# Kernel tuning notes

Hardware: AMD Instinct MI355X
Metric: run time of the kernel (lower is better)

## Reference

```python
import jax, jax.numpy as jnp
import numpy as np
from jax.ops import segment_sum, segment_max

N_NODES = 50000
N_EDGES = 800000
B = 1024            # number of graphs
NODE_DIM = 21
ESM_DIM = 480
TAB_DIM = 7
H = 128             # hidden_dim
LSTM_H = H // 2     # 64 per direction
NEG_SLOPE = 0.2
BN_EPS = 1e-5


def setup_inputs() -> dict:
    key = jax.random.key(0)
    ks = iter(jax.random.split(key, 48))
    r = lambda shape, s=0.05: (s * jax.random.normal(next(ks), shape)).astype(jnp.float32)
    inp = {
        'x': jax.random.normal(next(ks), (N_NODES, NODE_DIM), dtype=jnp.float32),
        'edge_index': jax.random.randint(next(ks), (2, N_EDGES), 0, N_NODES, dtype=jnp.int64),
        'batch': jnp.sort(jax.random.randint(next(ks), (N_NODES,), 0, B, dtype=jnp.int64)),
        'esm_emb': jax.random.normal(next(ks), (B, ESM_DIM), dtype=jnp.float32),
        'tab_feats': jax.random.normal(next(ks), (B, TAB_DIM), dtype=jnp.float32),
        # GATConv 1 (heads=1)
        'gat1_W': r((H, NODE_DIM)), 'gat1_asrc': r((H,)), 'gat1_adst': r((H,)), 'gat1_b': r((H,)),
        # GATConv 2
        'gat2_W': r((H, H)), 'gat2_asrc': r((H,)), 'gat2_adst': r((H,)), 'gat2_b': r((H,)),
        # Bidirectional LSTM (seq_len=1, so a single cell step per direction)
        'lstm_Wih_f': r((4 * LSTM_H, ESM_DIM)), 'lstm_Whh_f': r((4 * LSTM_H, LSTM_H)),
        'lstm_bih_f': r((4 * LSTM_H,)), 'lstm_bhh_f': r((4 * LSTM_H,)),
        'lstm_Wih_r': r((4 * LSTM_H, ESM_DIM)), 'lstm_Whh_r': r((4 * LSTM_H, LSTM_H)),
        'lstm_bih_r': r((4 * LSTM_H,)), 'lstm_bhh_r': r((4 * LSTM_H,)),
        # tabular net
        'tab_W': r((64, TAB_DIM)), 'tab_b': r((64,)), 'tab_bn_g': jnp.ones((64,), jnp.float32), 'tab_bn_b': jnp.zeros((64,), jnp.float32),
        # fusion head
        'fus1_W': r((256, 320)), 'fus1_b': r((256,)), 'fus_bn_g': jnp.ones((256,), jnp.float32), 'fus_bn_b': jnp.zeros((256,), jnp.float32),
        'fus2_W': r((128, 256)), 'fus2_b': r((128,)),
        'fus3_W': r((1, 128)), 'fus3_b': r((1,)),
    }
    return inp


def _gat(h_in, src, dst, W, a_src, a_dst, bias):
    # PyG GATConv, heads=1, concat=True, self-loops already appended.
    h = h_in @ W.T                                  # [N, H]
    alpha_s = h @ a_src                             # [N]
    alpha_d = h @ a_dst                             # [N]
    e = jax.nn.leaky_relu(alpha_s[src] + alpha_d[dst], NEG_SLOPE)  # [E]
    m = segment_max(e, dst, num_segments=N_NODES)   # stable softmax per target
    ex = jnp.exp(e - m[dst])
    den = segment_sum(ex, dst, num_segments=N_NODES)
    coef = ex / (den[dst] + 1e-16)
    out = segment_sum(coef[:, None] * h[src], dst, num_segments=N_NODES)
    return out + bias


def _bn(x, g, b):
    # BatchNorm1d in training mode: biased batch statistics
    mu = jnp.mean(x, axis=0)
    var = jnp.var(x, axis=0)
    return (x - mu) * jax.lax.rsqrt(var + BN_EPS) * g + b


def _lstm_step(x, Wih, Whh, bih, bhh):
    # single step with zero initial (h, c); Whh term vanishes but kept for fidelity
    g = x @ Wih.T + bih + jnp.zeros((x.shape[0], Whh.shape[1]), x.dtype) @ Whh.T + bhh
    i, f, gg, o = jnp.split(g, 4, axis=1)           # PyTorch gate order i,f,g,o
    c = jax.nn.sigmoid(i) * jnp.tanh(gg)
    return jax.nn.sigmoid(o) * jnp.tanh(c)


def reference(x, edge_index, batch, esm_emb, tab_feats,
              gat1_W, gat1_asrc, gat1_adst, gat1_b,
              gat2_W, gat2_asrc, gat2_adst, gat2_b,
              lstm_Wih_f, lstm_Whh_f, lstm_bih_f, lstm_bhh_f,
              lstm_Wih_r, lstm_Whh_r, lstm_bih_r, lstm_bhh_r,
              tab_W, tab_b, tab_bn_g, tab_bn_b,
              fus1_W, fus1_b, fus_bn_g, fus_bn_b,
              fus2_W, fus2_b, fus3_W, fus3_b):
    sl = jnp.arange(N_NODES, dtype=edge_index.dtype)
    src = jnp.concatenate([edge_index[0], sl])      # add_self_loops=True default
    dst = jnp.concatenate([edge_index[1], sl])

    h1 = jax.nn.relu(_gat(x, src, dst, gat1_W, gat1_asrc, gat1_adst, gat1_b))
    h2 = jax.nn.relu(_gat(h1, src, dst, gat2_W, gat2_asrc, gat2_adst, gat2_b))

    counts = segment_sum(jnp.ones((N_NODES,), h2.dtype), batch, num_segments=B)
    graph_embed = segment_sum(h2, batch, num_segments=B) / jnp.maximum(counts, 1.0)[:, None]

    # bilstm over seq_len=1: output at last (only) step = concat(fwd, bwd)
    h_f = _lstm_step(esm_emb, lstm_Wih_f, lstm_Whh_f, lstm_bih_f, lstm_bhh_f)
    h_r = _lstm_step(esm_emb, lstm_Wih_r, lstm_Whh_r, lstm_bih_r, lstm_bhh_r)
    seq_embed = jnp.concatenate([h_f, h_r], axis=1)  # [B, 128]

    tab_embed = jax.nn.relu(_bn(tab_feats @ tab_W.T + tab_b, tab_bn_g, tab_bn_b))

    z = jnp.concatenate([graph_embed, seq_embed, tab_embed], axis=1)  # [B, 320]
    z = jax.nn.relu(_bn(z @ fus1_W.T + fus1_b, fus_bn_g, fus_bn_b))   # dropout: identity (eval)
    z = jax.nn.relu(z @ fus2_W.T + fus2_b)
    return z @ fus3_W.T + fus3_b                     # [B, 1]
```

## Files before the change

kernel.cpp:

```cpp
#include <hip/hip_runtime.h>
#include <hip/hip_bf16.h>

#define N_NODES 50000
#define N_PAD   50048
#define N_EDGES 800000
#define E_TOT   850000
#define NB      1024
#define ESM_DIM 480
#define HD      128
#define NBUCK   196
#define CAP     5120
#define EPB     1661
#define SC_BLK  512
#define CVT_BLK 256
#define BND_BLK 196
#define WC_BLK  16
#define TAB_BLK 4
#define G1B     782
#define LSTM_B  96
#define LG      384
#define AGG_GRID 12500
#define NL_BLK  512

typedef short short8 __attribute__((ext_vector_type(8)));
typedef unsigned short ushort8 __attribute__((ext_vector_type(8)));
typedef float f32x4 __attribute__((ext_vector_type(4)));

__device__ __forceinline__ float bf2f(unsigned int u) {
    union { unsigned int i; float f; } c; c.i = u << 16; return c.f;
}
__device__ __forceinline__ unsigned short f2bf(float f) {
    union { float f; unsigned int i; } c; c.f = f;
    unsigned int i = c.i;
    return (unsigned short)((i + 0x7FFFu + ((i >> 16) & 1u)) >> 16);
}
__device__ __forceinline__ void split2(float v, unsigned short& h, unsigned short& l) {
    h = f2bf(v);
    l = f2bf(v - bf2f(h));
}


__device__ void dev_scatter(const int* __restrict__ ei, int* __restrict__ gcur,
                            int* __restrict__ pairs, int blk) {
    __shared__ int hist[NBUCK];
    int t = threadIdx.x;
    for (int u = t; u < NBUCK; u += 256) hist[u] = 0;
    __syncthreads();
    int e0 = blk * EPB;
    int e1 = (e0 + EPB < E_TOT) ? e0 + EPB : E_TOT;
    for (int e = e0 + t; e < e1; e += 256) {
        int d = (e < N_EDGES) ? ei[N_EDGES + e] : (e - N_EDGES);
        atomicAdd(&hist[d >> 8], 1);
    }
    __syncthreads();
    for (int u = t; u < NBUCK; u += 256) {
        int c = hist[u];
        hist[u] = (c > 0) ? atomicAdd(&gcur[u], c) : 0;
    }
    __syncthreads();
    for (int e = e0 + t; e < e1; e += 256) {
        int s, d;
        if (e < N_EDGES) { s = ei[e]; d = ei[N_EDGES + e]; }
        else             { s = d = e - N_EDGES; }
        int bu = d >> 8;
        int pos = atomicAdd(&hist[bu], 1);
        pairs[bu * CAP + pos] = s | ((d & 255) << 16);
    }
}

__device__ void dev_cvt(const float* __restrict__ esm,
                        const float* __restrict__ Wf,
                        const float* __restrict__ Wr,
                        const float* __restrict__ W1,
                        unsigned short* __restrict__ esm_h, unsigned short* __restrict__ esm_l,
                        unsigned short* __restrict__ wg_h,  unsigned short* __restrict__ wg_l,
                        unsigned short* __restrict__ w1h,   unsigned short* __restrict__ w1l,
                        int blk) {
    int tid = blk * 256 + threadIdx.x;
    for (int u = tid; u < NB * 120; u += CVT_BLK * 256) {
        float4 v = ((const float4*)esm)[u];
        ushort4 h, l;
        split2(v.x, h.x, l.x); split2(v.y, h.y, l.y);
        split2(v.z, h.z, l.z); split2(v.w, h.w, l.w);
        ((ushort4*)esm_h)[u] = h; ((ushort4*)esm_l)[u] = l;
    }
    for (int u = tid; u < LG * 120; u += CVT_BLK * 256) {
        int n = u / 120, kk = u - n * 120;
        int rr = (n >= 192) ? n - 192 : n;
        const float* Ws = (n >= 192) ? Wr : Wf;
        int srow = (rr < 64) ? rr : rr + 64;
        float4 v = *(const float4*)&Ws[(size_t)srow * 480 + kk * 4];
        ushort4 h, l;
        split2(v.x, h.x, l.x); split2(v.y, h.y, l.y);
        split2(v.z, h.z, l.z); split2(v.w, h.w, l.w);
        ((ushort4*)wg_h)[u] = h; ((ushort4*)wg_l)[u] = l;
    }
    for (int u = tid; u < 128 * 32; u += CVT_BLK * 256) {
        int f = u >> 5, k = u & 31;
        float v = (k < 21) ? W1[f * 21 + k] : 0.f;
        unsigned short h, l;
        split2(v, h, l);
        w1h[u] = h; w1l[u] = l;
    }
}

__device__ void dev_tab4(const float* __restrict__ tf, const float* __restrict__ W,
                         const float* __restrict__ bias, const float* __restrict__ g,
                         const float* __restrict__ b, float* __restrict__ z, int blk) {
    __shared__ float ssum[16][16];
    __shared__ float ssq[16][16];
    int t = threadIdx.x;
    int rg = t >> 4, jl = t & 15;
    int j = blk * 16 + jl;
    float Wj[7];
#pragma unroll
    for (int k = 0; k < 7; ++k) Wj[k] = W[j * 7 + k];
    float bj = bias[j];
    float s = 0.f, q = 0.f;
    for (int rr = 0; rr < 64; ++rr) {
        int row = rg * 64 + rr;
        const float* xp = &tf[(size_t)row * 7];
        float a = bj;
#pragma unroll
        for (int k = 0; k < 7; ++k) a += xp[k] * Wj[k];
        s += a; q += a * a;
    }
    ssum[rg][jl] = s; ssq[rg][jl] = q;
    __syncthreads();
    for (int off = 8; off; off >>= 1) {
        if (rg < off) { ssum[rg][jl] += ssum[rg + off][jl]; ssq[rg][jl] += ssq[rg + off][jl]; }
        __syncthreads();
    }
    float mu = ssum[0][jl] * (1.f / 1024.f);
    float var = ssq[0][jl] * (1.f / 1024.f) - mu * mu;
    float sc = rsqrtf(var + 1e-5f) * g[j];
    float sh = b[j] - mu * sc;
    for (int rr = 0; rr < 64; ++rr) {
        int row = rg * 64 + rr;
        const float* xp = &tf[(size_t)row * 7];
        float a = bj;
#pragma unroll
        for (int k = 0; k < 7; ++k) a += xp[k] * Wj[k];
        z[(size_t)row * 320 + 256 + j] = fmaxf(a * sc + sh, 0.f);
    }
}

__global__ __launch_bounds__(256) void megaA(
        const int* __restrict__ ei, int* __restrict__ gcur, int* __restrict__ pairs,
        const float* __restrict__ esm, const float* __restrict__ Wih_f,
        const float* __restrict__ Wih_r, const float* __restrict__ gat1_W,
        unsigned short* __restrict__ esm_h, unsigned short* __restrict__ esm_l,
        unsigned short* __restrict__ wg_h,  unsigned short* __restrict__ wg_l,
        unsigned short* __restrict__ w1h,   unsigned short* __restrict__ w1l,
        const int* __restrict__ batch, int* __restrict__ gstart,
        const float* __restrict__ W2, unsigned short* __restrict__ Wb,
        const float* __restrict__ tf, const float* __restrict__ tab_W,
        const float* __restrict__ tab_b, const float* __restrict__ tab_g,
        const float* __restrict__ tab_bb, float* __restrict__ z) {
    int b = blockIdx.x, t = threadIdx.x;
    if (b < SC_BLK) {
        dev_scatter(ei, gcur, pairs, b);
    } else if (b < SC_BLK + CVT_BLK) {
        dev_cvt(esm, Wih_f, Wih_r, gat1_W, esm_h, esm_l, wg_h, wg_l, w1h, w1l, b - SC_BLK);
    } else if (b < SC_BLK + CVT_BLK + BND_BLK) {
        int i = (b - (SC_BLK + CVT_BLK)) * 256 + t;
        if (i >= N_NODES) return;
        int bb = batch[i];
        int bp = (i == 0) ? -1 : batch[i - 1];
        for (int g = bp + 1; g <= bb; ++g) gstart[g] = i;
        if (i == N_NODES - 1)
            for (int g = bb + 1; g <= NB; ++g) gstart[g] = N_NODES;
    } else if (b < SC_BLK + CVT_BLK + BND_BLK + WC_BLK) {
        int i = (b - (SC_BLK + CVT_BLK + BND_BLK)) * 256 + t;
        if (i >= 128 * 32) return;
        float4 v = ((const float4*)W2)[i];
        ((ushort4*)Wb)[i] = make_ushort4(f2bf(v.x), f2bf(v.y), f2bf(v.z), f2bf(v.w));
    } else {
        dev_tab4(tf, tab_W, tab_b, tab_g, tab_bb, z,
                 b - (SC_BLK + CVT_BLK + BND_BLK + WC_BLK));
    }
}


__device__ __forceinline__ float sigmoidf_(float x) { return 1.f / (1.f + __expf(-x)); }

__device__ void dev_gat1_mfma(const float* __restrict__ X,
                              const unsigned short* __restrict__ w1h,
                              const unsigned short* __restrict__ w1l,
                              const float* __restrict__ asrc, const float* __restrict__ adst,
                              unsigned short* __restrict__ out,
                              float* __restrict__ alpha_s, float* __restrict__ alpha_d,
                              int blk) {
    int t = threadIdx.x;
    int wid = t >> 6, L = t & 63, quad = L >> 4, lo = L & 15;
    int m0 = blk * 64 + wid * 16;
    int row = m0 + lo;
    const float* xr = X + (size_t)row * 21;
    int kbase = quad * 8;
    bool valid = row < N_NODES;
    float xv[8];
#pragma unroll
    for (int j = 0; j < 8; ++j) {
        int k = kbase + j;
        xv[j] = (valid && k < 21) ? xr[k] : 0.f;
    }
    short8 ah, al;
#pragma unroll
    for (int j = 0; j < 8; ++j) {
        unsigned short h, l;
        split2(xv[j], h, l);
        ah[j] = (short)h; al[j] = (short)l;
    }
    float as_p[4] = {0.f, 0.f, 0.f, 0.f};
    float ad_p[4] = {0.f, 0.f, 0.f, 0.f};
#pragma unroll
    for (int ft = 0; ft < 8; ++ft) {
        short8 bh = *(const short8*)&w1h[(ft * 16 + lo) * 32 + kbase];
        short8 bl = *(const short8*)&w1l[(ft * 16 + lo) * 32 + kbase];
        f32x4 acc = {0.f, 0.f, 0.f, 0.f};
        acc = __builtin_amdgcn_mfma_f32_16x16x32_bf16(ah, bh, acc, 0, 0, 0);
        acc = __builtin_amdgcn_mfma_f32_16x16x32_bf16(al, bh, acc, 0, 0, 0);
        acc = __builtin_amdgcn_mfma_f32_16x16x32_bf16(ah, bl, acc, 0, 0, 0);
        float asv = asrc[ft * 16 + lo];
        float adv = adst[ft * 16 + lo];
#pragma unroll
        for (int r = 0; r < 4; ++r) {
            int m = m0 + quad * 4 + r;
            out[(size_t)m * HD + ft * 16 + lo] = f2bf(acc[r]);
            as_p[r] += acc[r] * asv;
            ad_p[r] += acc[r] * adv;
        }
    }
#pragma unroll
    for (int off = 1; off < 16; off <<= 1) {
#pragma unroll
        for (int r = 0; r < 4; ++r) {
            as_p[r] += __shfl_xor(as_p[r], off);
            ad_p[r] += __shfl_xor(ad_p[r], off);
        }
    }
    if (lo == 0) {
#pragma unroll
        for (int r = 0; r < 4; ++r) {
            int m = m0 + quad * 4 + r;
            if (m < N_NODES) { alpha_s[m] = as_p[r]; alpha_d[m] = ad_p[r]; }
        }
    }
}

__device__ void dev_lstm_mfma(const unsigned short* __restrict__ Ah,
                              const unsigned short* __restrict__ Al,
                              const unsigned short* __restrict__ Bh,
                              const unsigned short* __restrict__ Bl,
                              float* __restrict__ G, int blk) {
    __shared__ unsigned short Bsh[64][104];
    __shared__ unsigned short Bsl[64][104];
    int t = threadIdx.x;
    int wid = t >> 6, L = t & 63, quad = L >> 4, lo = L & 15;
    int nt = blk % 6, mt = blk / 6;
    int m0 = mt * 64 + wid * 16;
    int n0 = nt * 64;
    f32x4 accs[4];
#pragma unroll
    for (int ft = 0; ft < 4; ++ft) accs[ft] = (f32x4){0.f, 0.f, 0.f, 0.f};
    const unsigned short* arh = Ah + (size_t)(m0 + lo) * ESM_DIM;
    const unsigned short* arl = Al + (size_t)(m0 + lo) * ESM_DIM;
    for (int c = 0; c < 5; ++c) {
        int k0c = c * 96;
        short8 ah[3], al[3];
#pragma unroll
        for (int ks = 0; ks < 3; ++ks) {
            ah[ks] = *(const short8*)&arh[k0c + ks * 32 + quad * 8];
            al[ks] = *(const short8*)&arl[k0c + ks * 32 + quad * 8];
        }
#pragma unroll
        for (int u = 0; u < 3; ++u) {
            int li = u * 2048 + t * 8;
            int row = li / 96, col = li % 96;
            *(ushort8*)&Bsh[row][col] =
                *(const ushort8*)&Bh[(size_t)(n0 + row) * ESM_DIM + k0c + col];
            *(ushort8*)&Bsl[row][col] =
                *(const ushort8*)&Bl[(size_t)(n0 + row) * ESM_DIM + k0c + col];
        }
        __syncthreads();
#pragma unroll
        for (int ks = 0; ks < 3; ++ks) {
#pragma unroll
            for (int ft = 0; ft < 4; ++ft) {
                short8 bh = *(const short8*)&Bsh[ft * 16 + lo][ks * 32 + quad * 8];
                short8 bl = *(const short8*)&Bsl[ft * 16 + lo][ks * 32 + quad * 8];
                accs[ft] = __builtin_amdgcn_mfma_f32_16x16x32_bf16(ah[ks], bh, accs[ft], 0, 0, 0);
                accs[ft] = __builtin_amdgcn_mfma_f32_16x16x32_bf16(al[ks], bh, accs[ft], 0, 0, 0);
                accs[ft] = __builtin_amdgcn_mfma_f32_16x16x32_bf16(ah[ks], bl, accs[ft], 0, 0, 0);
            }
        }
        __syncthreads();
    }
#pragma unroll
    for (int ft = 0; ft < 4; ++ft) {
#pragma unroll
        for (int r = 0; r < 4; ++r)
            G[(size_t)(m0 + quad * 4 + r) * LG + n0 + ft * 16 + lo] = accs[ft][r];
    }
}

__global__ __launch_bounds__(256) void megaB(
        const int* __restrict__ gcur, const int* __restrict__ pairs,
        int* __restrict__ row_beg, int* __restrict__ row_end, int* __restrict__ csr_src,
        const float* __restrict__ x,
        const unsigned short* __restrict__ w1h, const unsigned short* __restrict__ w1l,
        const float* __restrict__ gat1_as, const float* __restrict__ gat1_ad,
        unsigned short* __restrict__ h0, float* __restrict__ alpha_s, float* __restrict__ alpha_d,
        const unsigned short* __restrict__ esm_h, const unsigned short* __restrict__ esm_l,
        const unsigned short* __restrict__ wg_h,  const unsigned short* __restrict__ wg_l,
        float* __restrict__ g_lstm) {
    int b = blockIdx.x, t = threadIdx.x;
    if (b < NBUCK) {
        __shared__ int dc[256];
        __shared__ int wt[4];
        __shared__ int cur[256];
        int rs = b * CAP;
        int re = rs + gcur[b];
        dc[t] = 0;
        __syncthreads();
        for (int i = rs + t; i < re; i += 1024) {
            int i1 = i + 256, i2 = i + 512, i3 = i + 768;
            int p0 = pairs[i];
            int p1 = (i1 < re) ? pairs[i1] : 0;
            int p2 = (i2 < re) ? pairs[i2] : 0;
            int p3 = (i3 < re) ? pairs[i3] : 0;
            atomicAdd(&dc[p0 >> 16], 1);
            if (i1 < re) atomicAdd(&dc[p1 >> 16], 1);
            if (i2 < re) atomicAdd(&dc[p2 >> 16], 1);
            if (i3 < re) atomicAdd(&dc[p3 >> 16], 1);
        }
        __syncthreads();
        int v = dc[t];
        int lane = t & 63, wid = t >> 6;
        int sc = v;
#pragma unroll
        for (int off = 1; off < 64; off <<= 1) {
            int n = __shfl_up(sc, off);
            if (lane >= off) sc += n;
        }
        if (lane == 63) wt[wid] = sc;
        __syncthreads();
        int pref = 0;
        for (int ww = 0; ww < wid; ++ww) pref += wt[ww];
        int beg = rs + pref + sc - v;
        int node = b * 256 + t;
        if (node < N_NODES) { row_beg[node] = beg; row_end[node] = beg + v; }
        cur[t] = beg;
        __syncthreads();
        for (int i = rs + t; i < re; i += 1024) {
            int i1 = i + 256, i2 = i + 512, i3 = i + 768;
            int p0 = pairs[i];
            int p1 = (i1 < re) ? pairs[i1] : 0;
            int p2 = (i2 < re) ? pairs[i2] : 0;
            int p3 = (i3 < re) ? pairs[i3] : 0;
            int pos0 = atomicAdd(&cur[p0 >> 16], 1);
            csr_src[pos0] = p0 & 0xFFFF;
            if (i1 < re) { int pos = atomicAdd(&cur[p1 >> 16], 1); csr_src[pos] = p1 & 0xFFFF; }
            if (i2 < re) { int pos = atomicAdd(&cur[p2 >> 16], 1); csr_src[pos] = p2 & 0xFFFF; }
            if (i3 < re) { int pos = atomicAdd(&cur[p3 >> 16], 1); csr_src[pos] = p3 & 0xFFFF; }
        }
    } else if (b < NBUCK + LSTM_B) {
        dev_lstm_mfma(esm_h, esm_l, wg_h, wg_l, g_lstm, b - NBUCK);
    } else {
        dev_gat1_mfma(x, w1h, w1l, gat1_as, gat1_ad, h0, alpha_s, alpha_d,
                      b - (NBUCK + LSTM_B));
    }
}


__global__ __launch_bounds__(256) void gemm_mfma(const unsigned short* __restrict__ A,
                                                 const unsigned short* __restrict__ Wb,
                                                 const float* __restrict__ asrc,
                                                 const float* __restrict__ adst,
                                                 unsigned short* __restrict__ out,
                                                 float* __restrict__ alpha_s,
                                                 float* __restrict__ alpha_d, int M) {
    __shared__ unsigned short Wlds[128 * 136];
    int t = threadIdx.x;
    for (int u = t; u < 128 * 16; u += 256) {
        int row = u >> 4, seg = u & 15;
        *(ushort8*)&Wlds[row * 136 + seg * 8] = *(const ushort8*)&Wb[row * 128 + seg * 8];
    }
    __syncthreads();
    int wid = t >> 6, L = t & 63;
    int quad = L >> 4, lo = L & 15;
    int m0 = blockIdx.x * 64 + wid * 16;
    short8 afrag[4];
#pragma unroll
    for (int ch = 0; ch < 4; ++ch)
        afrag[ch] = *(const short8*)&A[(size_t)(m0 + lo) * HD + ch * 32 + quad * 8];
    float as_p[4] = {0.f, 0.f, 0.f, 0.f};
    float ad_p[4] = {0.f, 0.f, 0.f, 0.f};
#pragma unroll
    for (int ft = 0; ft < 8; ++ft) {
        f32x4 acc = {0.f, 0.f, 0.f, 0.f};
#pragma unroll
        for (int ch = 0; ch < 4; ++ch) {
            short8 b = *(const short8*)&Wlds[(ft * 16 + lo) * 136 + ch * 32 + quad * 8];
            acc = __builtin_amdgcn_mfma_f32_16x16x32_bf16(afrag[ch], b, acc, 0, 0, 0);
        }
        float asv = asrc[ft * 16 + lo];
        float adv = adst[ft * 16 + lo];
#pragma unroll
        for (int r = 0; r < 4; ++r) {
            int m = m0 + quad * 4 + r;
            if (m < M) out[(size_t)m * HD + ft * 16 + lo] = f2bf(acc[r]);
            as_p[r] += acc[r] * asv;
            ad_p[r] += acc[r] * adv;
        }
    }
#pragma unroll
    for (int off = 1; off < 16; off <<= 1) {
#pragma unroll
        for (int r = 0; r < 4; ++r) {
            as_p[r] += __shfl_xor(as_p[r], off);
            ad_p[r] += __shfl_xor(ad_p[r], off);
        }
    }
    if (lo == 0) {
#pragma unroll
        for (int r = 0; r < 4; ++r) {
            int m = m0 + quad * 4 + r;
            if (m < M) { alpha_s[m] = as_p[r]; alpha_d[m] = ad_p[r]; }
        }
    }
}


__global__ void gat_spmm(const unsigned short* __restrict__ h, const int* __restrict__ row_beg,
                         const int* __restrict__ row_end, const int* __restrict__ csr_src,
                         const float* __restrict__ alpha_s, const float* __restrict__ alpha_d,
                         const float* __restrict__ bias, unsigned short* __restrict__ outp,
                         const float* __restrict__ g_lstm,
                         const float* __restrict__ bihf, const float* __restrict__ bhhf,
                         const float* __restrict__ bihr, const float* __restrict__ bhhr,
                         float* __restrict__ z) {
    if (blockIdx.x >= AGG_GRID) {
        int idx = (blockIdx.x - AGG_GRID) * 256 + threadIdx.x;
        int bb = idx >> 7, jj = idx & 127;
        int dir = jj >> 6, j = jj & 63;
        const float* gb = g_lstm + (size_t)bb * LG + dir * 192;
        const float* bi = dir ? bihr : bihf;
        const float* bh = dir ? bhhr : bhhf;
        float gi = gb[j]        + bi[j]        + bh[j];
        float gg = gb[64 + j]   + bi[128 + j]  + bh[128 + j];
        float go = gb[128 + j]  + bi[192 + j]  + bh[192 + j];
        float c = sigmoidf_(gi) * tanhf(gg);
        z[(size_t)bb * 320 + 128 + jj] = sigmoidf_(go) * tanhf(c);
        return;
    }
    int w = (int)((blockIdx.x * (size_t)blockDim.x + threadIdx.x) >> 6);
    int lane = threadIdx.x & 63;
    if (w >= N_NODES) return;
    int grp = lane >> 4, l16 = lane & 15;
    int rs = row_beg[w], re = row_end[w];
    int deg = re - rs;
    float ad = alpha_d[w];
    float acc[8] = {0.f, 0.f, 0.f, 0.f, 0.f, 0.f, 0.f, 0.f};
    if (deg <= 64) {
        int s_reg = 0;
        float e = -1e30f;
        if (lane < deg) {
            s_reg = csr_src[rs + lane];
            float t0 = alpha_s[s_reg] + ad;
            e = (t0 > 0.f) ? t0 : 0.2f * t0;
        }
        float m = e;
#pragma unroll
        for (int off = 32; off; off >>= 1) m = fmaxf(m, __shfl_xor(m, off));
        float ex = (lane < deg) ? __expf(e - m) : 0.f;
        float den = ex;
#pragma unroll
        for (int off = 32; off; off >>= 1) den += __shfl_xor(den, off);
        float coef = ex / (den + 1e-16f);
        int i = rs + grp;
        for (; i + 12 < re; i += 16) {
            int idx = i - rs;
            float c0 = __shfl(coef, idx);       int s0 = __shfl(s_reg, idx);
            float c1 = __shfl(coef, idx + 4);   int s1 = __shfl(s_reg, idx + 4);
            float c2 = __shfl(coef, idx + 8);   int s2 = __shfl(s_reg, idx + 8);
            float c3 = __shfl(coef, idx + 12);  int s3 = __shfl(s_reg, idx + 12);
            ushort8 h0 = *(const ushort8*)&h[(size_t)s0 * HD + l16 * 8];
            ushort8 h1 = *(const ushort8*)&h[(size_t)s1 * HD + l16 * 8];
            ushort8 h2 = *(const ushort8*)&h[(size_t)s2 * HD + l16 * 8];
            ushort8 h3 = *(const ushort8*)&h[(size_t)s3 * HD + l16 * 8];
#pragma unroll
            for (int j = 0; j < 8; ++j) acc[j] += c0 * bf2f(h0[j]);
#pragma unroll
            for (int j = 0; j < 8; ++j) acc[j] += c1 * bf2f(h1[j]);
#pragma unroll
            for (int j = 0; j < 8; ++j) acc[j] += c2 * bf2f(h2[j]);
#pragma unroll
            for (int j = 0; j < 8; ++j) acc[j] += c3 * bf2f(h3[j]);
        }
        for (; i < re; i += 4) {
            int idx = i - rs;
            float c0 = __shfl(coef, idx);
            int   s0 = __shfl(s_reg, idx);
            ushort8 h0 = *(const ushort8*)&h[(size_t)s0 * HD + l16 * 8];
#pragma unroll
            for (int j = 0; j < 8; ++j) acc[j] += c0 * bf2f(h0[j]);
        }
    } else {
        float m = -1e30f;
        for (int i = rs + lane; i < re; i += 64) {
            int s = csr_src[i];
            float t0 = alpha_s[s] + ad;
            t0 = (t0 > 0.f) ? t0 : 0.2f * t0;
            m = fmaxf(m, t0);
        }
#pragma unroll
        for (int off = 32; off; off >>= 1) m = fmaxf(m, __shfl_xor(m, off));
        float den = 0.f;
        for (int i = rs + lane; i < re; i += 64) {
            int s = csr_src[i];
            float t0 = alpha_s[s] + ad;
            t0 = (t0 > 0.f) ? t0 : 0.2f * t0;
            den += __expf(t0 - m);
        }
#pragma unroll
        for (int off = 32; off; off >>= 1) den += __shfl_xor(den, off);
        float inv = 1.f / (den + 1e-16f);
        for (int i = rs + grp; i < re; i += 4) {
            int s = csr_src[i];
            float t0 = alpha_s[s] + ad;
            t0 = (t0 > 0.f) ? t0 : 0.2f * t0;
            float c = __expf(t0 - m) * inv;
            ushort8 hv = *(const ushort8*)&h[(size_t)s * HD + l16 * 8];
#pragma unroll
            for (int j = 0; j < 8; ++j) acc[j] += c * bf2f(hv[j]);
        }
    }
#pragma unroll
    for (int j = 0; j < 8; ++j) {
        acc[j] += __shfl_xor(acc[j], 16);
        acc[j] += __shfl_xor(acc[j], 32);
    }
    int f0 = l16 * 8 + grp * 2;
    float2 bv = *(const float2*)&bias[f0];
    float vx = fmaxf(acc[grp * 2]     + bv.x, 0.f);
    float vy = fmaxf(acc[grp * 2 + 1] + bv.y, 0.f);
    unsigned int pv = (unsigned int)f2bf(vx) | ((unsigned int)f2bf(vy) << 16);
    *(unsigned int*)&outp[(size_t)w * HD + f0] = pv;
}


__global__ void pool_kernel(const unsigned short* __restrict__ h, const int* __restrict__ start,
                            float* __restrict__ z) {
    int w = (int)((blockIdx.x * (size_t)blockDim.x + threadIdx.x) >> 6);
    int lane = threadIdx.x & 63;
    if (w >= NB) return;
    int grp = lane >> 4, l16 = lane & 15;
    int s0 = start[w], s1 = start[w + 1];
    float acc[8] = {0.f, 0.f, 0.f, 0.f, 0.f, 0.f, 0.f, 0.f};
    int n = s0 + grp;
    for (; n + 4 < s1; n += 8) {
        ushort8 a = *(const ushort8*)&h[(size_t)n * HD + l16 * 8];
        ushort8 b = *(const ushort8*)&h[(size_t)(n + 4) * HD + l16 * 8];
#pragma unroll
        for (int j = 0; j < 8; ++j) acc[j] += bf2f(a[j]);
#pragma unroll
        for (int j = 0; j < 8; ++j) acc[j] += bf2f(b[j]);
    }
    if (n < s1) {
        ushort8 a = *(const ushort8*)&h[(size_t)n * HD + l16 * 8];
#pragma unroll
        for (int j = 0; j < 8; ++j) acc[j] += bf2f(a[j]);
    }
#pragma unroll
    for (int j = 0; j < 8; ++j) {
        acc[j] += __shfl_xor(acc[j], 16);
        acc[j] += __shfl_xor(acc[j], 32);
    }
    float inv = 1.f / fmaxf((float)(s1 - s0), 1.f);
    int f0 = l16 * 8 + grp * 2;
    *(float2*)&z[(size_t)w * 320 + f0] =
        make_float2(acc[grp * 2] * inv, acc[grp * 2 + 1] * inv);
}


__global__ __launch_bounds__(256) void fus1_mfma(const float* __restrict__ X,
                                                 const float* __restrict__ W1,
                                                 float* __restrict__ out,
                                                 float* __restrict__ colsum,
                                                 float* __restrict__ colsq) {
    __shared__ unsigned short Bsh[64][72];
    __shared__ unsigned short Bsl[64][72];
    __shared__ float cls[64], clq[64];
    int t = threadIdx.x;
    int wid = t >> 6, L = t & 63, quad = L >> 4, lo = L & 15;
    int m0 = blockIdx.x * 64 + wid * 16;
    int n0 = blockIdx.y * 64;
    if (t < 64) { cls[t] = 0.f; clq[t] = 0.f; }
    f32x4 accs[4];
#pragma unroll
    for (int ft = 0; ft < 4; ++ft) accs[ft] = (f32x4){0.f, 0.f, 0.f, 0.f};
    const float* ar = X + (size_t)(m0 + lo) * 320;
    for (int c = 0; c < 5; ++c) {
        int k0 = c * 64;
        short8 ah[2], al[2];
#pragma unroll
        for (int ks = 0; ks < 2; ++ks) {
            const float* ap = &ar[k0 + ks * 32 + quad * 8];
            float4 v0 = *(const float4*)ap;
            float4 v1 = *(const float4*)(ap + 4);
            float av[8] = {v0.x, v0.y, v0.z, v0.w, v1.x, v1.y, v1.z, v1.w};
#pragma unroll
            for (int j = 0; j < 8; ++j) {
                unsigned short hh, ll;
                split2(av[j], hh, ll);
                ah[ks][j] = (short)hh; al[ks][j] = (short)ll;
            }
        }
#pragma unroll
        for (int u = 0; u < 4; ++u) {
            int li = u * 256 + t;
            int row = li >> 4, col = (li & 15) * 4;
            float4 v = *(const float4*)&W1[(size_t)(n0 + row) * 320 + k0 + col];
            ushort4 hh, ll;
            split2(v.x, hh.x, ll.x); split2(v.y, hh.y, ll.y);
            split2(v.z, hh.z, ll.z); split2(v.w, hh.w, ll.w);
            *(ushort4*)&Bsh[row][col] = hh;
            *(ushort4*)&Bsl[row][col] = ll;
        }
        __syncthreads();
#pragma unroll
        for (int ks = 0; ks < 2; ++ks) {
#pragma unroll
            for (int ft = 0; ft < 4; ++ft) {
                short8 bh = *(const short8*)&Bsh[ft * 16 + lo][ks * 32 + quad * 8];
                short8 bl = *(const short8*)&Bsl[ft * 16 + lo][ks * 32 + quad * 8];
                accs[ft] = __builtin_amdgcn_mfma_f32_16x16x32_bf16(ah[ks], bh, accs[ft], 0, 0, 0);
                accs[ft] = __builtin_amdgcn_mfma_f32_16x16x32_bf16(al[ks], bh, accs[ft], 0, 0, 0);
                accs[ft] = __builtin_amdgcn_mfma_f32_16x16x32_bf16(ah[ks], bl, accs[ft], 0, 0, 0);
            }
        }
        __syncthreads();
    }
#pragma unroll
    for (int ft = 0; ft < 4; ++ft) {
        float s = 0.f, q = 0.f;
#pragma unroll
        for (int r = 0; r < 4; ++r) {
            float v = accs[ft][r];
            out[(size_t)(m0 + quad * 4 + r) * 256 + n0 + ft * 16 + lo] = v;
            s += v; q += v * v;
        }
        s += __shfl_xor(s, 16); s += __shfl_xor(s, 32);
        q += __shfl_xor(q, 16); q += __shfl_xor(q, 32);
        if (quad == 0) {
            atomicAdd(&cls[ft * 16 + lo], s);
            atomicAdd(&clq[ft * 16 + lo], q);
        }
    }
    __syncthreads();
    if (t < 64) {
        atomicAdd(&colsum[n0 + t], cls[t]);
        atomicAdd(&colsq[n0 + t],  clq[t]);
    }
}


__global__ __launch_bounds__(256) void fus2_mfma(const float* __restrict__ z1pre,
                                                 const float* __restrict__ colsum,
                                                 const float* __restrict__ colsq,
                                                 const float* __restrict__ fus_g,
                                                 const float* __restrict__ fus_bb,
                                                 const float* __restrict__ W2,
                                                 const float* __restrict__ b2,
                                                 const float* __restrict__ W3,
                                                 const float* __restrict__ b3,
                                                 float* __restrict__ out) {
    __shared__ unsigned short Bsh[128][72];
    __shared__ unsigned short Bsl[128][72];
    __shared__ float sc_[256], sh_[256];
    int t = threadIdx.x;
    {
        float mu = colsum[t] * (1.f / 1024.f);
        float var = colsq[t] * (1.f / 1024.f) - mu * mu;
        float s = rsqrtf(var + 1e-5f) * fus_g[t];
        sc_[t] = s;
        sh_[t] = fus_bb[t] - mu * s;
    }
    __syncthreads();
    int wid = t >> 6, L = t & 63, quad = L >> 4, lo = L & 15;
    int m0 = blockIdx.x * 64 + wid * 16;
    f32x4 accs[8];
#pragma unroll
    for (int ft = 0; ft < 8; ++ft) accs[ft] = (f32x4){0.f, 0.f, 0.f, 0.f};
    const float* ar = z1pre + (size_t)(m0 + lo) * 256;
    for (int c = 0; c < 4; ++c) {
        int k0 = c * 64;
        short8 ah[2], al[2];
#pragma unroll
        for (int ks = 0; ks < 2; ++ks) {
            int kb = k0 + ks * 32 + quad * 8;
            float4 v0 = *(const float4*)&ar[kb];
            float4 v1 = *(const float4*)&ar[kb + 4];
            float av[8] = {v0.x, v0.y, v0.z, v0.w, v1.x, v1.y, v1.z, v1.w};
#pragma unroll
            for (int j = 0; j < 8; ++j) {
                float xv = fmaxf(av[j] * sc_[kb + j] + sh_[kb + j], 0.f);
                unsigned short hh, ll;
                split2(xv, hh, ll);
                ah[ks][j] = (short)hh; al[ks][j] = (short)ll;
            }
        }
#pragma unroll
        for (int u = 0; u < 8; ++u) {
            int li = u * 256 + t;
            int row = li >> 4, col = (li & 15) * 4;
            float4 v = *(const float4*)&W2[(size_t)row * 256 + k0 + col];
            ushort4 hh, ll;
            split2(v.x, hh.x, ll.x); split2(v.y, hh.y, ll.y);
            split2(v.z, hh.z, ll.z); split2(v.w, hh.w, ll.w);
            *(ushort4*)&Bsh[row][col] = hh;
            *(ushort4*)&Bsl[row][col] = ll;
        }
        __syncthreads();
#pragma unroll
        for (int ks = 0; ks < 2; ++ks) {
#pragma unroll
            for (int ft = 0; ft < 8; ++ft) {
                short8 bh = *(const short8*)&Bsh[ft * 16 + lo][ks * 32 + quad * 8];
                short8 bl = *(const short8*)&Bsl[ft * 16 + lo][ks * 32 + quad * 8];
                accs[ft] = __builtin_amdgcn_mfma_f32_16x16x32_bf16(ah[ks], bh, accs[ft], 0, 0, 0);
                accs[ft] = __builtin_amdgcn_mfma_f32_16x16x32_bf16(al[ks], bh, accs[ft], 0, 0, 0);
                accs[ft] = __builtin_amdgcn_mfma_f32_16x16x32_bf16(ah[ks], bl, accs[ft], 0, 0, 0);
            }
        }
        __syncthreads();
    }
    float b3v = b3[0];
    float b2v[8], w3v[8];
#pragma unroll
    for (int ft = 0; ft < 8; ++ft) {
        int col = ft * 16 + lo;
        b2v[ft] = b2[col];
        w3v[ft] = W3[col];
    }
#pragma unroll
    for (int r = 0; r < 4; ++r) {
        float rsum = 0.f;
#pragma unroll
        for (int ft = 0; ft < 8; ++ft)
            rsum += fmaxf(accs[ft][r] + b2v[ft], 0.f) * w3v[ft];
        rsum += __shfl_xor(rsum, 1);
        rsum += __shfl_xor(rsum, 2);
        rsum += __shfl_xor(rsum, 4);
        rsum += __shfl_xor(rsum, 8);
        if (lo == 0) out[m0 + quad * 4 + r] = rsum + b3v;
    }
}


extern "C" void kernel_launch(void* const* d_in, const int* in_sizes, int n_in,
                              void* d_out, int out_size, void* d_ws, size_t ws_size,
                              hipStream_t stream) {
    const float* x        = (const float*)d_in[0];
    const int*   ei       = (const int*)d_in[1];
    const int*   batch    = (const int*)d_in[2];
    const float* esm      = (const float*)d_in[3];
    const float* tabf     = (const float*)d_in[4];
    const float* gat1_W   = (const float*)d_in[5];
    const float* gat1_as  = (const float*)d_in[6];
    const float* gat1_ad  = (const float*)d_in[7];
    const float* gat1_b   = (const float*)d_in[8];
    const float* gat2_W   = (const float*)d_in[9];
    const float* gat2_as  = (const float*)d_in[10];
    const float* gat2_ad  = (const float*)d_in[11];
    const float* gat2_b   = (const float*)d_in[12];
    const float* Wih_f    = (const float*)d_in[13];
    const float* bih_f    = (const float*)d_in[15];
    const float* bhh_f    = (const float*)d_in[16];
    const float* Wih_r    = (const float*)d_in[17];
    const float* bih_r    = (const float*)d_in[19];
    const float* bhh_r    = (const float*)d_in[20];
    const float* tab_W    = (const float*)d_in[21];
    const float* tab_b    = (const float*)d_in[22];
    const float* tab_g    = (const float*)d_in[23];
    const float* tab_bb   = (const float*)d_in[24];
    const float* fus1_W   = (const float*)d_in[25];
    const float* fus_g    = (const float*)d_in[27];
    const float* fus_bb   = (const float*)d_in[28];
    const float* fus2_W   = (const float*)d_in[29];
    const float* fus2_b   = (const float*)d_in[30];
    const float* fus3_W   = (const float*)d_in[31];
    const float* fus3_b   = (const float*)d_in[32];
    float* out = (float*)d_out;

    char* ws = (char*)d_ws;
    size_t off = 0;
    auto alloc = [&](size_t bytes) -> char* {
        char* p = ws + off;
        off += (bytes + 255) & ~(size_t)255;
        return p;
    };
    unsigned short* h0_bf = (unsigned short*)alloc((size_t)N_PAD * HD * 2);
    unsigned short* hA_bf = (unsigned short*)alloc((size_t)N_PAD * HD * 2);
    unsigned short* h2_bf = (unsigned short*)alloc((size_t)N_PAD * HD * 2);
    unsigned short* h_act = (unsigned short*)alloc((size_t)N_NODES * HD * 2);
    float* alpha_s = (float*)alloc((size_t)N_NODES * 4);
    float* alpha_d = (float*)alloc((size_t)N_NODES * 4);
    unsigned short* w2bf = (unsigned short*)alloc((size_t)HD * HD * 2);
    int*   row_beg = (int*)alloc((size_t)N_NODES * 4);
    int*   row_end = (int*)alloc((size_t)N_NODES * 4);
    int*   csr_src = (int*)alloc((size_t)NBUCK * CAP * 4);
    int*   pairs   = (int*)alloc((size_t)NBUCK * CAP * 4);
    int*   gstart  = (int*)alloc((size_t)(NB + 1) * 4);
    float* z1pre   = (float*)alloc((size_t)NB * 256 * 4);
    float* z       = (float*)alloc((size_t)NB * 320 * 4);
    float* g_lstm  = (float*)alloc((size_t)NB * LG * 4);
    unsigned short* esm_h = (unsigned short*)alloc((size_t)NB * ESM_DIM * 2);
    unsigned short* esm_l = (unsigned short*)alloc((size_t)NB * ESM_DIM * 2);
    unsigned short* wg_h  = (unsigned short*)alloc((size_t)LG * ESM_DIM * 2);
    unsigned short* wg_l  = (unsigned short*)alloc((size_t)LG * ESM_DIM * 2);
    unsigned short* w1h   = (unsigned short*)alloc((size_t)128 * 32 * 2);
    unsigned short* w1l   = (unsigned short*)alloc((size_t)128 * 32 * 2);
    int*   gcur    = (int*)alloc((size_t)NBUCK * 4);
    float* colsum  = (float*)alloc((size_t)256 * 4);
    float* colsq   = (float*)alloc((size_t)256 * 4);
    size_t zero_len = (size_t)((char*)colsq + 256 * 4 - (char*)gcur);
    hipMemsetAsync(gcur, 0, zero_len, stream);

    megaA<<<SC_BLK + CVT_BLK + BND_BLK + WC_BLK + TAB_BLK, 256, 0, stream>>>(
        ei, gcur, pairs, esm, Wih_f, Wih_r, gat1_W,
        esm_h, esm_l, wg_h, wg_l, w1h, w1l,
        batch, gstart, gat2_W, w2bf,
        tabf, tab_W, tab_b, tab_g, tab_bb, z);

    megaB<<<NBUCK + LSTM_B + G1B, 256, 0, stream>>>(
        gcur, pairs, row_beg, row_end, csr_src,
        x, w1h, w1l, gat1_as, gat1_ad, h0_bf, alpha_s, alpha_d,
        esm_h, esm_l, wg_h, wg_l, g_lstm);

    gat_spmm<<<AGG_GRID + NL_BLK, 256, 0, stream>>>(h0_bf, row_beg, row_end, csr_src,
                                                    alpha_s, alpha_d, gat1_b, hA_bf,
                                                    g_lstm, bih_f, bhh_f, bih_r, bhh_r, z);

    gemm_mfma<<<N_PAD / 64, 256, 0, stream>>>(hA_bf, w2bf, gat2_as, gat2_ad,
                                              h2_bf, alpha_s, alpha_d, N_NODES);

    gat_spmm<<<AGG_GRID, 256, 0, stream>>>(h2_bf, row_beg, row_end, csr_src,
                                           alpha_s, alpha_d, gat2_b, h_act,
                                           g_lstm, bih_f, bhh_f, bih_r, bhh_r, z);

    pool_kernel<<<(NB + 3) / 4, 256, 0, stream>>>(h_act, gstart, z);

    fus1_mfma<<<dim3(16, 4), 256, 0, stream>>>(z, fus1_W, z1pre, colsum, colsq);

    fus2_mfma<<<16, 256, 0, stream>>>(z1pre, colsum, colsq, fus_g, fus_bb,
                                      fus2_W, fus2_b, fus3_W, fus3_b, out);

    (void)in_sizes; (void)n_in; (void)out_size; (void)ws_size;
}
```

Before: 279.7 us.

## Fuse mean pooling into second GAT aggregation via atomics, retune scatter blocks

Layer-2 aggregation now does graph mean pooling itself. Each block stages its four output rows in shared memory, pre-scales them by 1/count, merges runs of rows that belong to the same graph and atomically adds the result into z. This drops the separate pool kernel and the bf16 activation buffer it read and wrote, at the cost of float atomics and a block-wide sync per block. z is now zeroed by the memset, and atomic summation makes the pooled result order-dependent. The tail gather loop is also unrolled by two, and the edge-scatter stage uses half as many blocks with twice the edges each.

```diff
diff --git a/kernel.cpp b/kernel.cpp
--- a/kernel.cpp
+++ b/kernel.cpp
@@ -10,8 +10,8 @@
 #define HD      128
 #define NBUCK   196
 #define CAP     5120
-#define EPB     1661
-#define SC_BLK  512
+#define EPB     3321
+#define SC_BLK  256
 #define CVT_BLK 256
 #define BND_BLK 196
 #define WC_BLK  16
@@ -439,7 +439,9 @@
                          const float* __restrict__ g_lstm,
                          const float* __restrict__ bihf, const float* __restrict__ bhhf,
                          const float* __restrict__ bihr, const float* __restrict__ bhhr,
-                         float* __restrict__ z) {
+                         float* __restrict__ z,
+                         const int* __restrict__ batch, const int* __restrict__ gstart,
+                         int do_pool) {
     if (blockIdx.x >= AGG_GRID) {
         int idx = (blockIdx.x - AGG_GRID) * 256 + threadIdx.x;
         int bb = idx >> 7, jj = idx & 127;
@@ -453,6 +455,14 @@
         float c = sigmoidf_(gi) * tanhf(gg);
         z[(size_t)bb * 320 + 128 + jj] = sigmoidf_(go) * tanhf(c);
         return;
+    }
+    __shared__ float rowbuf[4][128];
+    __shared__ int   gids[4];
+    __shared__ float invs[4];
+    if (do_pool && threadIdx.x < 4) {
+        int g = batch[blockIdx.x * 4 + threadIdx.x];
+        gids[threadIdx.x] = g;
+        invs[threadIdx.x] = 1.f / fmaxf((float)(gstart[g + 1] - gstart[g]), 1.f);
     }
     int w = (int)((blockIdx.x * (size_t)blockDim.x + threadIdx.x) >> 6);
     int lane = threadIdx.x & 63;
@@ -498,7 +508,18 @@
 #pragma unroll
             for (int j = 0; j < 8; ++j) acc[j] += c3 * bf2f(h3[j]);
         }
-        for (; i < re; i += 4) {
+        for (; i + 4 < re; i += 8) {
+            int idx = i - rs;
+            float c0 = __shfl(coef, idx);       int s0 = __shfl(s_reg, idx);
+            float c1 = __shfl(coef, idx + 4);   int s1 = __shfl(s_reg, idx + 4);
+            ushort8 h0 = *(const ushort8*)&h[(size_t)s0 * HD + l16 * 8];
+            ushort8 h1 = *(const ushort8*)&h[(size_t)s1 * HD + l16 * 8];
+#pragma unroll
+            for (int j = 0; j < 8; ++j) acc[j] += c0 * bf2f(h0[j]);
+#pragma unroll
+            for (int j = 0; j < 8; ++j) acc[j] += c1 * bf2f(h1[j]);
+        }
+        if (i < re) {
             int idx = i - rs;
             float c0 = __shfl(coef, idx);
             int   s0 = __shfl(s_reg, idx);
@@ -545,42 +566,29 @@
     float2 bv = *(const float2*)&bias[f0];
     float vx = fmaxf(acc[grp * 2]     + bv.x, 0.f);
     float vy = fmaxf(acc[grp * 2 + 1] + bv.y, 0.f);
-    unsigned int pv = (unsigned int)f2bf(vx) | ((unsigned int)f2bf(vy) << 16);
-    *(unsigned int*)&outp[(size_t)w * HD + f0] = pv;
-}
-
-
-__global__ void pool_kernel(const unsigned short* __restrict__ h, const int* __restrict__ start,
-                            float* __restrict__ z) {
-    int w = (int)((blockIdx.x * (size_t)blockDim.x + threadIdx.x) >> 6);
-    int lane = threadIdx.x & 63;
-    if (w >= NB) return;
-    int grp = lane >> 4, l16 = lane & 15;
-    int s0 = start[w], s1 = start[w + 1];
-    float acc[8] = {0.f, 0.f, 0.f, 0.f, 0.f, 0.f, 0.f, 0.f};
-    int n = s0 + grp;
-    for (; n + 4 < s1; n += 8) {
-        ushort8 a = *(const ushort8*)&h[(size_t)n * HD + l16 * 8];
-        ushort8 b = *(const ushort8*)&h[(size_t)(n + 4) * HD + l16 * 8];
-#pragma unroll
-        for (int j = 0; j < 8; ++j) acc[j] += bf2f(a[j]);
-#pragma unroll
-        for (int j = 0; j < 8; ++j) acc[j] += bf2f(b[j]);
-    }
-    if (n < s1) {
-        ushort8 a = *(const ushort8*)&h[(size_t)n * HD + l16 * 8];
-#pragma unroll
-        for (int j = 0; j < 8; ++j) acc[j] += bf2f(a[j]);
-    }
-#pragma unroll
-    for (int j = 0; j < 8; ++j) {
-        acc[j] += __shfl_xor(acc[j], 16);
-        acc[j] += __shfl_xor(acc[j], 32);
-    }
-    float inv = 1.f / fmaxf((float)(s1 - s0), 1.f);
-    int f0 = l16 * 8 + grp * 2;
-    *(float2*)&z[(size_t)w * 320 + f0] =
-        make_float2(acc[grp * 2] * inv, acc[grp * 2 + 1] * inv);
+    unsigned short bx = f2bf(vx), by = f2bf(vy);
+    if (!do_pool) {
+        unsigned int pv = (unsigned int)bx | ((unsigned int)by << 16);
+        *(unsigned int*)&outp[(size_t)w * HD + f0] = pv;
+        return;
+    }
+    int wl = threadIdx.x >> 6;
+    rowbuf[wl][f0]     = bf2f((unsigned int)bx);
+    rowbuf[wl][f0 + 1] = bf2f((unsigned int)by);
+    __syncthreads();
+    if (threadIdx.x < 128) {
+        int c = threadIdx.x;
+        int   gprev = gids[0];
+        float val = rowbuf[0][c] * invs[0];
+#pragma unroll
+        for (int r = 1; r < 4; ++r) {
+            int g = gids[r];
+            float v = rowbuf[r][c] * invs[r];
+            if (g == gprev) { val += v; }
+            else { atomicAdd(&z[(size_t)gprev * 320 + c], val); gprev = g; val = v; }
+        }
+        atomicAdd(&z[(size_t)gprev * 320 + c], val);
+    }
 }
 
 
@@ -804,7 +812,6 @@
     unsigned short* h0_bf = (unsigned short*)alloc((size_t)N_PAD * HD * 2);
     unsigned short* hA_bf = (unsigned short*)alloc((size_t)N_PAD * HD * 2);
     unsigned short* h2_bf = (unsigned short*)alloc((size_t)N_PAD * HD * 2);
-    unsigned short* h_act = (unsigned short*)alloc((size_t)N_NODES * HD * 2);
     float* alpha_s = (float*)alloc((size_t)N_NODES * 4);
     float* alpha_d = (float*)alloc((size_t)N_NODES * 4);
     unsigned short* w2bf = (unsigned short*)alloc((size_t)HD * HD * 2);
@@ -814,7 +821,6 @@
     int*   pairs   = (int*)alloc((size_t)NBUCK * CAP * 4);
     int*   gstart  = (int*)alloc((size_t)(NB + 1) * 4);
     float* z1pre   = (float*)alloc((size_t)NB * 256 * 4);
-    float* z       = (float*)alloc((size_t)NB * 320 * 4);
     float* g_lstm  = (float*)alloc((size_t)NB * LG * 4);
     unsigned short* esm_h = (unsigned short*)alloc((size_t)NB * ESM_DIM * 2);
     unsigned short* esm_l = (unsigned short*)alloc((size_t)NB * ESM_DIM * 2);
@@ -822,11 +828,12 @@
     unsigned short* wg_l  = (unsigned short*)alloc((size_t)LG * ESM_DIM * 2);
     unsigned short* w1h   = (unsigned short*)alloc((size_t)128 * 32 * 2);
     unsigned short* w1l   = (unsigned short*)alloc((size_t)128 * 32 * 2);
+    float* z       = (float*)alloc((size_t)NB * 320 * 4);
     int*   gcur    = (int*)alloc((size_t)NBUCK * 4);
     float* colsum  = (float*)alloc((size_t)256 * 4);
     float* colsq   = (float*)alloc((size_t)256 * 4);
-    size_t zero_len = (size_t)((char*)colsq + 256 * 4 - (char*)gcur);
-    hipMemsetAsync(gcur, 0, zero_len, stream);
+    size_t zero_len = (size_t)((char*)colsq + 256 * 4 - (char*)z);
+    hipMemsetAsync(z, 0, zero_len, stream);
 
     megaA<<<SC_BLK + CVT_BLK + BND_BLK + WC_BLK + TAB_BLK, 256, 0, stream>>>(
         ei, gcur, pairs, esm, Wih_f, Wih_r, gat1_W,
@@ -841,16 +848,16 @@
 
     gat_spmm<<<AGG_GRID + NL_BLK, 256, 0, stream>>>(h0_bf, row_beg, row_end, csr_src,
                                                     alpha_s, alpha_d, gat1_b, hA_bf,
-                                                    g_lstm, bih_f, bhh_f, bih_r, bhh_r, z);
+                                                    g_lstm, bih_f, bhh_f, bih_r, bhh_r, z,
+                                                    batch, gstart, 0);
 
     gemm_mfma<<<N_PAD / 64, 256, 0, stream>>>(hA_bf, w2bf, gat2_as, gat2_ad,
                                               h2_bf, alpha_s, alpha_d, N_NODES);
 
     gat_spmm<<<AGG_GRID, 256, 0, stream>>>(h2_bf, row_beg, row_end, csr_src,
-                                           alpha_s, alpha_d, gat2_b, h_act,
-                                           g_lstm, bih_f, bhh_f, bih_r, bhh_r, z);
-
-    pool_kernel<<<(NB + 3) / 4, 256, 0, stream>>>(h_act, gstart, z);
+                                           alpha_s, alpha_d, gat2_b, hA_bf ,
+                                           g_lstm, bih_f, bhh_f, bih_r, bhh_r, z,
+                                           batch, gstart, 1);
 
     fus1_mfma<<<dim3(16, 4), 256, 0, stream>>>(z, fus1_W, z1pre, colsum, colsq);
 
```

Result: no change. 275.6 us (-1.5%).
